# Performance work log

Hardware: AMD Instinct MI355X
Metric: run time of the kernel (lower is better)

## Reference

```python
import jax, jax.numpy as jnp
import numpy as np

IN, OUT, R = 512, 512, 4
H = (IN + OUT) * R + OUT  # 4608, LSTM hidden size


def setup_inputs() -> dict:
    key = jax.random.key(0)
    ks = jax.random.split(key, 8)
    B = 256
    x = jax.random.normal(ks[0], (B, IN), dtype=jnp.float32)
    h0 = jax.random.normal(ks[1], (B, H), dtype=jnp.float32)
    c0 = jax.random.normal(ks[2], (B, H), dtype=jnp.float32)
    s_ih = 1.0 / np.sqrt(H)
    W_ih = jax.random.uniform(ks[3], (4 * H, IN), dtype=jnp.float32, minval=-s_ih, maxval=s_ih)
    W_hh = jax.random.uniform(ks[4], (4 * H, H), dtype=jnp.float32, minval=-s_ih, maxval=s_ih)
    b_ih = jax.random.uniform(ks[5], (4 * H,), dtype=jnp.float32, minval=-s_ih, maxval=s_ih)
    b_hh = jax.random.uniform(ks[6], (4 * H,), dtype=jnp.float32, minval=-s_ih, maxval=s_ih)
    initial_weight = jax.random.normal(ks[7], (1, OUT, IN), dtype=jnp.float32)
    initial_bias = jnp.zeros((1, OUT), dtype=jnp.float32)
    return {"x": x, "h0": h0, "c0": c0, "W_ih": W_ih, "W_hh": W_hh,
            "b_ih": b_ih, "b_hh": b_hh,
            "initial_weight": initial_weight, "initial_bias": initial_bias}


def reference(x, h0, c0, W_ih, W_hh, b_ih, b_hh, initial_weight, initial_bias):
    B = x.shape[0]
    # Batched LSTMCell (the per-sample python loop in the original is
    # mathematically identical to one batched cell).  PyTorch gate order: i,f,g,o.
    gates = x @ W_ih.T + b_ih + h0 @ W_hh.T + b_hh  # [B, 4H]
    i, f, g, o = jnp.split(gates, 4, axis=-1)
    c_new = jax.nn.sigmoid(f) * c0 + jax.nn.sigmoid(i) * jnp.tanh(g)
    h_new = jax.nn.sigmoid(o) * jnp.tanh(c_new)  # [B, H]
    # Low-rank per-sample weight deltas
    dw1 = h_new[:, : OUT * R].reshape(B, OUT, R)
    dw2 = h_new[:, OUT * R: OUT * R + IN * R].reshape(B, R, IN)
    db = h_new[:, OUT * R + IN * R:]  # [B, OUT]
    weight = initial_weight + jnp.einsum('bor,bri->boi', dw1, dw2)  # [B, OUT, IN]
    bias = initial_bias + db  # [B, OUT]
    y = jnp.einsum('bi,boi->bo', x, weight) + bias
    return (y, h_new, c_new)
```

## Files before the change

kernel.cpp:

```cpp
#include <hip/hip_runtime.h>

#define B_DIM 256
#define H_DIM 4608
#define K_X   512
#define K_TOT 5120
#define KT    32
#define NSTEP (K_TOT / KT)
#define LDA   40

typedef __attribute__((ext_vector_type(8))) short  short8;
typedef __attribute__((ext_vector_type(4))) float  floatx4;

static __device__ __forceinline__ unsigned pkbf(float a, float b){
  unsigned ua = (__float_as_uint(a) + 0x8000u) >> 16;
  unsigned ub = (__float_as_uint(b) + 0x8000u) & 0xFFFF0000u;
  return ua | ub;
}

static __device__ __forceinline__ float sigm(float v){
  return 1.0f / (1.0f + __expf(-v));
}
static __device__ __forceinline__ float tanh_fast(float v){
  float ax = fabsf(v);
  float e  = __expf(-2.0f * ax);
  float t  = (1.0f - e) / (1.0f + e);
  return copysignf(t, v);
}

__global__ __launch_bounds__(256, 2) void lstm_gates_kernel(
    const float* __restrict__ x,   const float* __restrict__ h0,
    const float* __restrict__ c0,
    const float* __restrict__ Wih, const float* __restrict__ Whh,
    const float* __restrict__ bih, const float* __restrict__ bhh,
    float* __restrict__ outH, float* __restrict__ outC)
{
  __shared__ __align__(16) unsigned short As[B_DIM * LDA];
  __shared__ __align__(16) unsigned short Bs[64 * LDA];

  const int t   = threadIdx.x;
  const int j0  = blockIdx.x * 16;
  const int w   = t >> 6;
  const int l   = t & 63;
  const int q   = l >> 4;
  const int col = l & 15;
  const int jj  = j0 + col;

  const int arow = t >> 2;
  const int k8   = (t & 3) * 8;
  const int nloc = t >> 2;
  const int gate = nloc >> 4;
  const int jl   = nloc & 15;
  const long wrowg = (long)gate * H_DIM + j0 + jl;

  long offAx[4], offAh[4];
  #pragma unroll
  for (int rep = 0; rep < 4; ++rep){
    int row = rep * 64 + arow;
    offAx[rep] = (long)row * K_X   + k8;
    offAh[rep] = (long)row * H_DIM + k8;
  }
  const long offBx = wrowg * K_X   + k8;
  const long offBh = wrowg * H_DIM + k8;

  floatx4 acc[4][4];
  #pragma unroll
  for (int nt = 0; nt < 4; ++nt){
    float bsum = bih[nt * H_DIM + jj] + bhh[nt * H_DIM + jj];
    floatx4 v = {bsum, bsum, bsum, bsum};
    #pragma unroll
    for (int mt = 0; mt < 4; ++mt) acc[mt][nt] = v;
  }

  floatx4 pa[4][2];
  floatx4 pb[2];

  auto load_tile = [&](int ko){
    if (ko < K_X){
      #pragma unroll
      for (int rep = 0; rep < 4; ++rep){
        const float* p = x + offAx[rep] + ko;
        pa[rep][0] = *(const floatx4*)p;
        pa[rep][1] = *(const floatx4*)(p + 4);
      }
      const float* pB = Wih + offBx + ko;
      pb[0] = *(const floatx4*)pB;
      pb[1] = *(const floatx4*)(pB + 4);
    } else {
      const int kh = ko - K_X;
      #pragma unroll
      for (int rep = 0; rep < 4; ++rep){
        const float* p = h0 + offAh[rep] + kh;
        pa[rep][0] = *(const floatx4*)p;
        pa[rep][1] = *(const floatx4*)(p + 4);
      }
      const float* pB = Whh + offBh + kh;
      pb[0] = *(const floatx4*)pB;
      pb[1] = *(const floatx4*)(pB + 4);
    }
  };

  load_tile(0);

  const int wrow = w * 64;
  const int aoff = (wrow + col) * LDA + q * 8;
  const int boff = col * LDA + q * 8;

  for (int kt = 0; kt < NSTEP; ++kt){
    __syncthreads();
    #pragma unroll
    for (int rep = 0; rep < 4; ++rep){
      uint4 wv;
      wv.x = pkbf(pa[rep][0].x, pa[rep][0].y);
      wv.y = pkbf(pa[rep][0].z, pa[rep][0].w);
      wv.z = pkbf(pa[rep][1].x, pa[rep][1].y);
      wv.w = pkbf(pa[rep][1].z, pa[rep][1].w);
      *(uint4*)&As[(rep * 64 + arow) * LDA + k8] = wv;
    }
    {
      uint4 wv;
      wv.x = pkbf(pb[0].x, pb[0].y);
      wv.y = pkbf(pb[0].z, pb[0].w);
      wv.z = pkbf(pb[1].x, pb[1].y);
      wv.w = pkbf(pb[1].z, pb[1].w);
      *(uint4*)&Bs[nloc * LDA + k8] = wv;
    }
    __syncthreads();

    if (kt + 1 < NSTEP) load_tile((kt + 1) * KT);

    short8 af[4], bf[4];
    #pragma unroll
    for (int mt = 0; mt < 4; ++mt)
      af[mt] = *(const short8*)&As[aoff + mt * 16 * LDA];
    #pragma unroll
    for (int nt = 0; nt < 4; ++nt)
      bf[nt] = *(const short8*)&Bs[boff + nt * 16 * LDA];
    #pragma unroll
    for (int mt = 0; mt < 4; ++mt)
      #pragma unroll
      for (int nt = 0; nt < 4; ++nt)
        acc[mt][nt] = __builtin_amdgcn_mfma_f32_16x16x32_bf16(af[mt], bf[nt], acc[mt][nt], 0, 0, 0);
  }

  #pragma unroll
  for (int mt = 0; mt < 4; ++mt){
    #pragma unroll
    for (int r = 0; r < 4; ++r){
      int brow = wrow + mt * 16 + q * 4 + r;
      float iv = acc[mt][0][r];
      float fv = acc[mt][1][r];
      float gv = acc[mt][2][r];
      float ov = acc[mt][3][r];
      float cp = c0[(long)brow * H_DIM + jj];
      float cn = sigm(fv) * cp + sigm(iv) * tanh_fast(gv);
      float hn = sigm(ov) * tanh_fast(cn);
      outH[(long)brow * H_DIM + jj] = hn;
      outC[(long)brow * H_DIM + jj] = cn;
    }
  }
}

__global__ __launch_bounds__(256) void y_kernel(
    const float* __restrict__ x, const float* __restrict__ hnew,
    const float* __restrict__ W0, const float* __restrict__ b0,
    float* __restrict__ y)
{
  __shared__ float xs[512];
  __shared__ float zs[4];
  const int b = blockIdx.x;
  const int t = threadIdx.x;
  const int w = t >> 6;
  const int l = t & 63;

  const float* xrow = x + (long)b * 512;
  xs[t]       = xrow[t];
  xs[t + 256] = xrow[t + 256];
  __syncthreads();

  const float* hrow = hnew + (long)b * H_DIM;

  {
    const float* d2 = hrow + 2048 + w * 512;
    float p = 0.f;
    #pragma unroll
    for (int j = 0; j < 8; ++j)
      p += d2[l + 64 * j] * xs[l + 64 * j];
    #pragma unroll
    for (int off = 32; off > 0; off >>= 1)
      p += __shfl_down(p, off);
    if (l == 0) zs[w] = p;
  }
  __syncthreads();
  const float z0 = zs[0], z1 = zs[1], z2 = zs[2], z3 = zs[3];

  for (int oo = 0; oo < 128; ++oo){
    int o = w * 128 + oo;
    const float* wr = W0 + (long)o * 512;
    float p = 0.f;
    #pragma unroll
    for (int j = 0; j < 8; ++j)
      p += wr[l + 64 * j] * xs[l + 64 * j];
    #pragma unroll
    for (int off = 32; off > 0; off >>= 1)
      p += __shfl_down(p, off);
    if (l == 0){
      float4 d1 = *(const float4*)&hrow[o * 4];
      float r = p + b0[o] + hrow[4096 + o]
              + d1.x * z0 + d1.y * z1 + d1.z * z2 + d1.w * z3;
      y[(long)b * 512 + o] = r;
    }
  }
}

extern "C" void kernel_launch(void* const* d_in, const int* in_sizes, int n_in,
                              void* d_out, int out_size, void* d_ws, size_t ws_size,
                              hipStream_t stream)
{
  const float* x   = (const float*)d_in[0];
  const float* h0  = (const float*)d_in[1];
  const float* c0  = (const float*)d_in[2];
  const float* Wih = (const float*)d_in[3];
  const float* Whh = (const float*)d_in[4];
  const float* bih = (const float*)d_in[5];
  const float* bhh = (const float*)d_in[6];
  const float* W0  = (const float*)d_in[7];
  const float* b0  = (const float*)d_in[8];

  float* out  = (float*)d_out;
  float* y    = out;
  float* outH = out + 131072;
  float* outC = out + 131072 + 1179648;

  hipLaunchKernelGGL(lstm_gates_kernel, dim3(288), dim3(256), 0, stream,
                     x, h0, c0, Wih, Whh, bih, bhh, outH, outC);
  hipLaunchKernelGGL(y_kernel, dim3(256), dim3(256), 0, stream,
                     x, outH, W0, b0, y);
}
```

Before: 728.6 us.

## Pre-convert activations to bf16, pipeline B tiles, and move y computation to MFMA

Adds a conversion kernel that packs x and h0 into a bf16 workspace once, so each gates block no longer re-reads and re-converts the full fp32 activation matrix. The gates kernel reads its A fragments directly from that buffer, double-buffers swizzled weight tiles in LDS with a four-deep register prefetch, and replaces syncthreads with raw barriers. It also computes the dw2·x reduction in its epilogue through atomics. The y kernel becomes a bf16 MFMA GEMM over W0, which costs an extra launch, workspace traffic, atomic contention, and a lower-precision W0 product.

New measurement: 677.5 us. -7.0%, faster.

```diff
diff --git a/kernel.cpp b/kernel.cpp
--- a/kernel.cpp
+++ b/kernel.cpp
@@ -4,22 +4,24 @@
 #define H_DIM 4608
 #define K_X   512
 #define K_TOT 5120
-#define KT    32
-#define NSTEP (K_TOT / KT)
-#define LDA   40
+#define NSTEP 160
 
 typedef __attribute__((ext_vector_type(8))) short  short8;
 typedef __attribute__((ext_vector_type(4))) float  floatx4;
+
+#define BAR() do { \
+  __builtin_amdgcn_sched_barrier(0); \
+  asm volatile("s_waitcnt lgkmcnt(0)" ::: "memory"); \
+  __builtin_amdgcn_s_barrier(); \
+  __builtin_amdgcn_sched_barrier(0); \
+} while (0)
 
 static __device__ __forceinline__ unsigned pkbf(float a, float b){
   unsigned ua = (__float_as_uint(a) + 0x8000u) >> 16;
   unsigned ub = (__float_as_uint(b) + 0x8000u) & 0xFFFF0000u;
   return ua | ub;
 }
-
-static __device__ __forceinline__ float sigm(float v){
-  return 1.0f / (1.0f + __expf(-v));
-}
+static __device__ __forceinline__ float sigm(float v){ return 1.0f / (1.0f + __expf(-v)); }
 static __device__ __forceinline__ float tanh_fast(float v){
   float ax = fabsf(v);
   float e  = __expf(-2.0f * ax);
@@ -27,40 +29,58 @@
   return copysignf(t, v);
 }
 
+__global__ __launch_bounds__(256) void conv_kernel(
+    const float* __restrict__ x, const float* __restrict__ h0,
+    unsigned short* __restrict__ Abf, float* __restrict__ z)
+{
+  const int t = threadIdx.x;
+  if (blockIdx.x == 0) ((float4*)z)[t] = make_float4(0.f, 0.f, 0.f, 0.f);
+  const long e = ((long)blockIdx.x * 256 + t) * 8;
+  const int  b = (int)(e / K_TOT);
+  const int  k = (int)(e - (long)b * K_TOT);
+  const float* src = (k < K_X) ? (x + (long)b * K_X + k)
+                               : (h0 + (long)b * H_DIM + (k - K_X));
+  float4 v0 = *(const float4*)src;
+  float4 v1 = *(const float4*)(src + 4);
+  uint4 wv;
+  wv.x = pkbf(v0.x, v0.y); wv.y = pkbf(v0.z, v0.w);
+  wv.z = pkbf(v1.x, v1.y); wv.w = pkbf(v1.z, v1.w);
+  *(uint4*)(Abf + e) = wv;
+}
+
 __global__ __launch_bounds__(256, 2) void lstm_gates_kernel(
-    const float* __restrict__ x,   const float* __restrict__ h0,
+    const unsigned short* __restrict__ Abf,
+    const float* __restrict__ x,
     const float* __restrict__ c0,
     const float* __restrict__ Wih, const float* __restrict__ Whh,
     const float* __restrict__ bih, const float* __restrict__ bhh,
-    float* __restrict__ outH, float* __restrict__ outC)
-{
-  __shared__ __align__(16) unsigned short As[B_DIM * LDA];
-  __shared__ __align__(16) unsigned short Bs[64 * LDA];
-
-  const int t   = threadIdx.x;
-  const int j0  = blockIdx.x * 16;
-  const int w   = t >> 6;
-  const int l   = t & 63;
-  const int q   = l >> 4;
-  const int col = l & 15;
-  const int jj  = j0 + col;
-
-  const int arow = t >> 2;
-  const int k8   = (t & 3) * 8;
-  const int nloc = t >> 2;
-  const int gate = nloc >> 4;
-  const int jl   = nloc & 15;
+    float* __restrict__ outH, float* __restrict__ outC,
+    float* __restrict__ z)
+{
+  __shared__ __align__(16) unsigned short Bs[2][64 * 32];
+
+  const int t    = threadIdx.x;
+  const int j0   = blockIdx.x * 16;
+  const int w    = t >> 6;
+  const int l    = t & 63;
+  const int q    = l >> 4;
+  const int col  = l & 15;
+  const int jj   = j0 + col;
+  const int wrow = w * 64;
+
+  const long aBase = (long)(wrow + col) * K_TOT + q * 8;
+
+  const int  rB   = t >> 2;
+  const int  cB   = t & 3;
+  const int  gate = rB >> 4;
+  const int  jl   = rB & 15;
   const long wrowg = (long)gate * H_DIM + j0 + jl;
-
-  long offAx[4], offAh[4];
-  #pragma unroll
-  for (int rep = 0; rep < 4; ++rep){
-    int row = rep * 64 + arow;
-    offAx[rep] = (long)row * K_X   + k8;
-    offAh[rep] = (long)row * H_DIM + k8;
-  }
-  const long offBx = wrowg * K_X   + k8;
-  const long offBh = wrowg * H_DIM + k8;
+  const float* __restrict__ pWx = Wih + wrowg * K_X   + cB * 8;
+  const float* __restrict__ pWh = Whh + wrowg * H_DIM + cB * 8;
+
+  char* ldsBase = (char*)&Bs[0][0];
+  const int bwByte = rB  * 64 + ((cB ^ ((rB  >> 1) & 3)) << 4);
+  const int brByte = col * 64 + ((q  ^ ((col >> 1) & 3)) << 4);
 
   floatx4 acc[4][4];
   #pragma unroll
@@ -71,143 +91,161 @@
     for (int mt = 0; mt < 4; ++mt) acc[mt][nt] = v;
   }
 
-  floatx4 pa[4][2];
-  floatx4 pb[2];
-
-  auto load_tile = [&](int ko){
-    if (ko < K_X){
-      #pragma unroll
-      for (int rep = 0; rep < 4; ++rep){
-        const float* p = x + offAx[rep] + ko;
-        pa[rep][0] = *(const floatx4*)p;
-        pa[rep][1] = *(const floatx4*)(p + 4);
-      }
-      const float* pB = Wih + offBx + ko;
-      pb[0] = *(const floatx4*)pB;
-      pb[1] = *(const floatx4*)(pB + 4);
-    } else {
-      const int kh = ko - K_X;
-      #pragma unroll
-      for (int rep = 0; rep < 4; ++rep){
-        const float* p = h0 + offAh[rep] + kh;
-        pa[rep][0] = *(const floatx4*)p;
-        pa[rep][1] = *(const floatx4*)(p + 4);
-      }
-      const float* pB = Whh + offBh + kh;
-      pb[0] = *(const floatx4*)pB;
-      pb[1] = *(const floatx4*)(pB + 4);
-    }
-  };
-
-  load_tile(0);
-
-  const int wrow = w * 64;
-  const int aoff = (wrow + col) * LDA + q * 8;
-  const int boff = col * LDA + q * 8;
-
-  for (int kt = 0; kt < NSTEP; ++kt){
-    __syncthreads();
-    #pragma unroll
-    for (int rep = 0; rep < 4; ++rep){
-      uint4 wv;
-      wv.x = pkbf(pa[rep][0].x, pa[rep][0].y);
-      wv.y = pkbf(pa[rep][0].z, pa[rep][0].w);
-      wv.z = pkbf(pa[rep][1].x, pa[rep][1].y);
-      wv.w = pkbf(pa[rep][1].z, pa[rep][1].w);
-      *(uint4*)&As[(rep * 64 + arow) * LDA + k8] = wv;
-    }
-    {
-      uint4 wv;
-      wv.x = pkbf(pb[0].x, pb[0].y);
-      wv.y = pkbf(pb[0].z, pb[0].w);
-      wv.z = pkbf(pb[1].x, pb[1].y);
-      wv.w = pkbf(pb[1].z, pb[1].w);
-      *(uint4*)&Bs[nloc * LDA + k8] = wv;
-    }
-    __syncthreads();
-
-    if (kt + 1 < NSTEP) load_tile((kt + 1) * KT);
-
-    short8 af[4], bf[4];
+  float4 pb[4][2];
+  short8 af0[4], af1[4];
+
+  auto issueB = [&](int kt, int slot){
+    const int ko = kt * 32;
+    const float* p = (ko < K_X) ? (pWx + ko) : (pWh + (ko - K_X));
+    pb[slot][0] = *(const float4*)p;
+    pb[slot][1] = *(const float4*)(p + 4);
+  };
+  auto writeB = [&](int slot, int buf){
+    uint4 wv;
+    wv.x = pkbf(pb[slot][0].x, pb[slot][0].y);
+    wv.y = pkbf(pb[slot][0].z, pb[slot][0].w);
+    wv.z = pkbf(pb[slot][1].x, pb[slot][1].y);
+    wv.w = pkbf(pb[slot][1].z, pb[slot][1].w);
+    *(uint4*)(ldsBase + buf * 4096 + bwByte) = wv;
+  };
+  auto loadA = [&](int kt, short8* af){
+    const unsigned short* p = Abf + (aBase + kt * 32);
     #pragma unroll
     for (int mt = 0; mt < 4; ++mt)
-      af[mt] = *(const short8*)&As[aoff + mt * 16 * LDA];
+      af[mt] = *(const short8*)(p + (long)mt * (16 * K_TOT));
+  };
+  auto mfmaStep = [&](int buf, const short8* af){
+    short8 bf[4];
     #pragma unroll
     for (int nt = 0; nt < 4; ++nt)
-      bf[nt] = *(const short8*)&Bs[boff + nt * 16 * LDA];
+      bf[nt] = *(const short8*)(ldsBase + buf * 4096 + brByte + nt * 1024);
     #pragma unroll
     for (int mt = 0; mt < 4; ++mt)
       #pragma unroll
       for (int nt = 0; nt < 4; ++nt)
         acc[mt][nt] = __builtin_amdgcn_mfma_f32_16x16x32_bf16(af[mt], bf[nt], acc[mt][nt], 0, 0, 0);
-  }
+  };
+
+  issueB(0, 0); issueB(1, 1); issueB(2, 2); issueB(3, 3);
+  loadA(0, af0);
+  writeB(0, 0);
+  BAR();
+
+  #pragma unroll 1
+  for (int k = 0; k < NSTEP; k += 4){
+    loadA(k + 1, af1);
+    if (k + 4 < NSTEP) issueB(k + 4, 0);
+    mfmaStep(0, af0);
+    writeB(1, 1);
+    BAR();
+    loadA(k + 2, af0);
+    if (k + 5 < NSTEP) issueB(k + 5, 1);
+    mfmaStep(1, af1);
+    writeB(2, 0);
+    BAR();
+    loadA(k + 3, af1);
+    if (k + 6 < NSTEP) issueB(k + 6, 2);
+    mfmaStep(0, af0);
+    writeB(3, 1);
+    BAR();
+    if (k + 4 < NSTEP) loadA(k + 4, af0);
+    if (k + 7 < NSTEP) issueB(k + 7, 3);
+    mfmaStep(1, af1);
+    if (k + 4 < NSTEP) writeB(0, 0);
+    BAR();
+  }
+
+  const bool isDw2 = (j0 >= 2048) && (j0 < 4096);
+  const int  rIdx  = (j0 - 2048) >> 9;
+  const int  i0    = (j0 - 2048) & 511;
 
   #pragma unroll
   for (int mt = 0; mt < 4; ++mt){
     #pragma unroll
-    for (int r = 0; r < 4; ++r){
-      int brow = wrow + mt * 16 + q * 4 + r;
-      float iv = acc[mt][0][r];
-      float fv = acc[mt][1][r];
-      float gv = acc[mt][2][r];
-      float ov = acc[mt][3][r];
+    for (int r2 = 0; r2 < 4; ++r2){
+      const int brow = wrow + mt * 16 + q * 4 + r2;
+      float iv = acc[mt][0][r2];
+      float fv = acc[mt][1][r2];
+      float gv = acc[mt][2][r2];
+      float ov = acc[mt][3][r2];
       float cp = c0[(long)brow * H_DIM + jj];
       float cn = sigm(fv) * cp + sigm(iv) * tanh_fast(gv);
       float hn = sigm(ov) * tanh_fast(cn);
       outH[(long)brow * H_DIM + jj] = hn;
       outC[(long)brow * H_DIM + jj] = cn;
+      if (isDw2){
+        float v = hn * x[(long)brow * K_X + i0 + col];
+        v += __shfl_xor(v, 1); v += __shfl_xor(v, 2);
+        v += __shfl_xor(v, 4); v += __shfl_xor(v, 8);
+        if (col == 0) atomicAdd(&z[brow * 4 + rIdx], v);
+      }
     }
   }
 }
 
 __global__ __launch_bounds__(256) void y_kernel(
-    const float* __restrict__ x, const float* __restrict__ hnew,
+    const unsigned short* __restrict__ Abf,
+    const float* __restrict__ hnew,
     const float* __restrict__ W0, const float* __restrict__ b0,
+    const float* __restrict__ z,
     float* __restrict__ y)
 {
-  __shared__ float xs[512];
-  __shared__ float zs[4];
-  const int b = blockIdx.x;
-  const int t = threadIdx.x;
-  const int w = t >> 6;
-  const int l = t & 63;
-
-  const float* xrow = x + (long)b * 512;
-  xs[t]       = xrow[t];
-  xs[t + 256] = xrow[t + 256];
+  __shared__ __align__(16) unsigned short Ws[16 * 512];
+  const int t    = threadIdx.x;
+  const int w    = t >> 6;
+  const int l    = t & 63;
+  const int q    = l >> 4;
+  const int col  = l & 15;
+  const int n0   = blockIdx.x * 16;
+  const int wrow = w * 64;
+
+  {
+    const int r  = t >> 4;
+    const int kc = (t & 15) * 32;
+    const float* src = W0 + (long)(n0 + r) * 512 + kc;
+    #pragma unroll
+    for (int j = 0; j < 4; ++j){
+      float4 a = *(const float4*)(src + j * 8);
+      float4 b = *(const float4*)(src + j * 8 + 4);
+      uint4 wv;
+      wv.x = pkbf(a.x, a.y); wv.y = pkbf(a.z, a.w);
+      wv.z = pkbf(b.x, b.y); wv.w = pkbf(b.z, b.w);
+      const int cch = (kc >> 3) + j;
+      const int sw  = cch ^ (r & 7);
+      *(uint4*)((char*)Ws + r * 1024 + sw * 16) = wv;
+    }
+  }
   __syncthreads();
 
-  const float* hrow = hnew + (long)b * H_DIM;
-
-  {
-    const float* d2 = hrow + 2048 + w * 512;
-    float p = 0.f;
-    #pragma unroll
-    for (int j = 0; j < 8; ++j)
-      p += d2[l + 64 * j] * xs[l + 64 * j];
-    #pragma unroll
-    for (int off = 32; off > 0; off >>= 1)
-      p += __shfl_down(p, off);
-    if (l == 0) zs[w] = p;
-  }
-  __syncthreads();
-  const float z0 = zs[0], z1 = zs[1], z2 = zs[2], z3 = zs[3];
-
-  for (int oo = 0; oo < 128; ++oo){
-    int o = w * 128 + oo;
-    const float* wr = W0 + (long)o * 512;
-    float p = 0.f;
-    #pragma unroll
-    for (int j = 0; j < 8; ++j)
-      p += wr[l + 64 * j] * xs[l + 64 * j];
-    #pragma unroll
-    for (int off = 32; off > 0; off >>= 1)
-      p += __shfl_down(p, off);
-    if (l == 0){
-      float4 d1 = *(const float4*)&hrow[o * 4];
-      float r = p + b0[o] + hrow[4096 + o]
-              + d1.x * z0 + d1.y * z1 + d1.z * z2 + d1.w * z3;
-      y[(long)b * 512 + o] = r;
+  const long aBase = (long)(wrow + col) * K_TOT + q * 8;
+  floatx4 acc[4];
+  #pragma unroll
+  for (int mt = 0; mt < 4; ++mt) acc[mt] = (floatx4){0.f, 0.f, 0.f, 0.f};
+
+  #pragma unroll 4
+  for (int ks = 0; ks < 16; ++ks){
+    const int sw = (ks * 4 + q) ^ (col & 7);
+    short8 bf = *(const short8*)((char*)Ws + col * 1024 + sw * 16);
+    #pragma unroll
+    for (int mt = 0; mt < 4; ++mt){
+      short8 af = *(const short8*)(Abf + aBase + ks * 32 + (long)mt * (16 * K_TOT));
+      acc[mt] = __builtin_amdgcn_mfma_f32_16x16x32_bf16(af, bf, acc[mt], 0, 0, 0);
+    }
+  }
+
+  const int   o  = n0 + col;
+  const float bo = b0[o];
+  #pragma unroll
+  for (int mt = 0; mt < 4; ++mt){
+    #pragma unroll
+    for (int r2 = 0; r2 < 4; ++r2){
+      const int brow = wrow + mt * 16 + q * 4 + r2;
+      const float* hr = hnew + (long)brow * H_DIM;
+      float4 d1 = *(const float4*)(hr + o * 4);
+      float4 zr = *(const float4*)(z + brow * 4);
+      float val = acc[mt][r2] + bo + hr[4096 + o]
+                + d1.x * zr.x + d1.y * zr.y + d1.z * zr.z + d1.w * zr.w;
+      y[(long)brow * 512 + o] = val;
     }
   }
 }
@@ -216,6 +254,7 @@
                               void* d_out, int out_size, void* d_ws, size_t ws_size,
                               hipStream_t stream)
 {
+  (void)in_sizes; (void)n_in; (void)out_size; (void)ws_size;
   const float* x   = (const float*)d_in[0];
   const float* h0  = (const float*)d_in[1];
   const float* c0  = (const float*)d_in[2];
@@ -231,8 +270,11 @@
   float* outH = out + 131072;
   float* outC = out + 131072 + 1179648;
 
+  unsigned short* Abf = (unsigned short*)d_ws;
+  float* z = (float*)((char*)d_ws + (size_t)B_DIM * K_TOT * 2);
+
+  hipLaunchKernelGGL(conv_kernel, dim3(640), dim3(256), 0, stream, x, h0, Abf, z);
   hipLaunchKernelGGL(lstm_gates_kernel, dim3(288), dim3(256), 0, stream,
-                     x, h0, c0, Wih, Whh, bih, bhh, outH, outC);
-  hipLaunchKernelGGL(y_kernel, dim3(256), dim3(256), 0, stream,
-                     x, outH, W0, b0, y);
-}
+                     Abf, x, c0, Wih, Whh, bih, bhh, outH, outC, z);
+  hipLaunchKernelGGL(y_kernel, dim3(32), dim3(256), 0, stream, Abf, outH, W0, b0, z, y);
+}
```
